# Kernel tuning notes

Hardware: AMD Instinct MI355X
Metric: run time of the kernel (lower is better)

The kernel has to match this reference:

```python
import jax, jax.numpy as jnp
import numpy as np
import math

D_RES, N_HEADS, D_HEAD, D_MLP = 1024, 16, 64, 4096
EPS = 1e-5
IGNORE = -100000.0


def setup_inputs() -> dict:
    key = jax.random.key(0)
    ks = jax.random.split(key, 8)
    std = 0.02
    return {
        "resid_pre": jax.random.normal(ks[0], (2, 2048, D_RES), dtype=jnp.float32),
        "ln1_w": jnp.ones((D_RES,), jnp.float32),
        "ln1_b": jnp.zeros((D_RES,), jnp.float32),
        "W_Q": jax.random.normal(ks[1], (N_HEADS, D_RES, D_HEAD), jnp.float32) * std,
        "b_Q": jnp.zeros((N_HEADS, D_HEAD), jnp.float32),
        "W_K": jax.random.normal(ks[2], (N_HEADS, D_RES, D_HEAD), jnp.float32) * std,
        "b_K": jnp.zeros((N_HEADS, D_HEAD), jnp.float32),
        "W_V": jax.random.normal(ks[3], (N_HEADS, D_RES, D_HEAD), jnp.float32) * std,
        "b_V": jnp.zeros((N_HEADS, D_HEAD), jnp.float32),
        "W_O": jax.random.normal(ks[4], (N_HEADS, D_HEAD, D_RES), jnp.float32) * std,
        "b_O": jnp.zeros((D_RES,), jnp.float32),
        "ln2_w": jnp.ones((D_RES,), jnp.float32),
        "ln2_b": jnp.zeros((D_RES,), jnp.float32),
        "W_in": jax.random.normal(ks[5], (D_RES, D_MLP), jnp.float32) * std,
        "b_in": jnp.zeros((D_MLP,), jnp.float32),
        "W_out": jax.random.normal(ks[6], (D_MLP, D_RES), jnp.float32) * std,
        "b_out": jnp.zeros((D_RES,), jnp.float32),
    }


def _layernorm(x, w, b):
    x = x - jnp.mean(x, axis=-1, keepdims=True)
    scale = jnp.sqrt(jnp.mean(x * x, axis=-1, keepdims=True) + EPS)
    return (x / scale) * w + b


def reference(resid_pre, ln1_w, ln1_b, W_Q, b_Q, W_K, b_K, W_V, b_V, W_O, b_O,
              ln2_w, ln2_b, W_in, b_in, W_out, b_out):
    x = _layernorm(resid_pre, ln1_w, ln1_b)  # [b,s,d]
    q = jnp.einsum('bsd,hde->bshe', x, W_Q) + b_Q
    k = jnp.einsum('bsd,hde->bshe', x, W_K) + b_K
    v = jnp.einsum('bsd,hde->bshe', x, W_V) + b_V
    scores = jnp.einsum('bqhe,bkhe->bhqk', q, k) / math.sqrt(D_HEAD)
    S = scores.shape[-1]
    mask = jnp.triu(jnp.ones((S, S), dtype=bool), k=1)
    scores = jnp.where(mask, IGNORE, scores)
    pattern = jax.nn.softmax(scores, axis=-1)
    z = jnp.einsum('bhqk,bkhe->bqhe', pattern, v)
    attn_out = jnp.einsum('bqhe,hed->bqd', z, W_O) + b_O
    resid_mid = resid_pre + attn_out
    y = _layernorm(resid_mid, ln2_w, ln2_b)
    pre = jnp.einsum('bsd,dm->bsm', y, W_in) + b_in
    post = jax.nn.gelu(pre, approximate=False)
    mlp_out = jnp.einsum('bsm,md->bsd', post, W_out) + b_out
    return resid_mid + mlp_out
```

## Files before the change

kernel.cpp:

```cpp
#include <hip/hip_runtime.h>
#include <cstddef>

typedef unsigned short u16;
using short8 = __attribute__((ext_vector_type(8))) short;
using f32x4  = __attribute__((ext_vector_type(4))) float;

__device__ __forceinline__ float bf2f(u16 u) {
  union { unsigned int i; float f; } v; v.i = ((unsigned int)u) << 16; return v.f;
}
__device__ __forceinline__ u16 f2bf(float f) {
  __bf16 h = (__bf16)f;
  return __builtin_bit_cast(unsigned short, h);
}

__device__ __forceinline__ void load_lds16(const u16* g, u16* l) {
  __builtin_amdgcn_global_load_lds((const __attribute__((address_space(1))) void*)g,
                                   (__attribute__((address_space(3))) void*)l, 16, 0, 0);
}

__global__ __launch_bounds__(256) void prep_k(const float* __restrict__ wq,
                                              const float* __restrict__ wk,
                                              const float* __restrict__ wv,
                                              const float* __restrict__ wo,
                                              const float* __restrict__ win,
                                              const float* __restrict__ wout,
                                              const float* __restrict__ bq,
                                              const float* __restrict__ bk,
                                              const float* __restrict__ bv,
                                              u16* __restrict__ wqkvT,
                                              u16* __restrict__ woT,
                                              u16* __restrict__ winT,
                                              u16* __restrict__ woutT,
                                              float* __restrict__ qkvBias) {
  __shared__ float tile[32][33];
  int id = blockIdx.x;
  int tx = threadIdx.x, ty = threadIdx.y;

  if (id == 12288) {
    int t = ty * 32 + tx;
#pragma unroll
    for (int i = 0; i < 12; ++i) {
      int idx = i * 256 + t;
      float v = (idx < 1024) ? bq[idx] : (idx < 2048) ? bk[idx - 1024] : bv[idx - 2048];
      qkvBias[idx] = v;
    }
    return;
  }

  const float* in; u16* out; int R, C, c0, r0;
  if (id < 3072) {
    int s = id >> 10, r = id & 1023;
    int h = r >> 6, tt = r & 63;
    const float* W = (s == 0) ? wq : (s == 1) ? wk : wv;
    in = W + h * 65536;
    out = wqkvT + (size_t)s * 1024 * 1024 + h * 64 * 1024;
    R = 1024; C = 64;
    c0 = (tt & 1) * 32; r0 = (tt >> 1) * 32;
  } else if (id < 4096) {
    int tt = id - 3072;
    in = wo; out = woT; R = 1024; C = 1024;
    c0 = (tt & 31) * 32; r0 = (tt >> 5) * 32;
  } else if (id < 8192) {
    int tt = id - 4096;
    in = win; out = winT; R = 1024; C = 4096;
    c0 = (tt & 127) * 32; r0 = (tt >> 7) * 32;
  } else {
    int tt = id - 8192;
    in = wout; out = woutT; R = 4096; C = 1024;
    c0 = (tt & 31) * 32; r0 = (tt >> 5) * 32;
  }

#pragma unroll
  for (int i = 0; i < 32; i += 8)
    tile[ty + i][tx] = in[(size_t)(r0 + ty + i) * C + c0 + tx];
  __syncthreads();
#pragma unroll
  for (int i = 0; i < 32; i += 8)
    out[(size_t)(c0 + ty + i) * R + r0 + tx] = f2bf(tile[tx][ty + i]);
}

__global__ __launch_bounds__(256) void transpose_v_k(const u16* __restrict__ qkv,
                                                     u16* __restrict__ vT) {
  __shared__ u16 tile[32][33];
  int bh = blockIdx.z;
  int b = bh >> 4, h = bh & 15;
  const u16* in = qkv + (size_t)b * 2048 * 3072 + 2048 + h * 64;
  u16* out = vT + (size_t)bh * 64 * 2048;
  int e0 = blockIdx.x * 32, s0 = blockIdx.y * 32;
  int tx = threadIdx.x, ty = threadIdx.y;
#pragma unroll
  for (int i = 0; i < 32; i += 8)
    tile[ty + i][tx] = in[(size_t)(s0 + ty + i) * 3072 + e0 + tx];
  __syncthreads();
#pragma unroll
  for (int i = 0; i < 32; i += 8)
    out[(size_t)(e0 + ty + i) * 2048 + s0 + tx] = tile[tx][ty + i];
}

__global__ __launch_bounds__(256) void ln_k(const float* __restrict__ inp,
                                            const float* __restrict__ w,
                                            const float* __restrict__ bias,
                                            u16* __restrict__ out) {
  __shared__ float red[2][4];
  int row = blockIdx.x, t = threadIdx.x;
  int wave = t >> 6, lane = t & 63;
  size_t base = (size_t)row * 1024 + t * 4;
  float4 f = *(const float4*)(inp + base);
  float v[4] = {f.x, f.y, f.z, f.w};
  float s = v[0] + v[1] + v[2] + v[3];
#pragma unroll
  for (int off = 32; off; off >>= 1) s += __shfl_xor(s, off, 64);
  if (lane == 0) red[0][wave] = s;
  __syncthreads();
  float mean = (red[0][0] + red[0][1] + red[0][2] + red[0][3]) * (1.f / 1024.f);
  float c[4]; float sq = 0.f;
#pragma unroll
  for (int j = 0; j < 4; ++j) { c[j] = v[j] - mean; sq += c[j] * c[j]; }
#pragma unroll
  for (int off = 32; off; off >>= 1) sq += __shfl_xor(sq, off, 64);
  if (lane == 0) red[1][wave] = sq;
  __syncthreads();
  float var = (red[1][0] + red[1][1] + red[1][2] + red[1][3]) * (1.f / 1024.f);
  float inv = 1.f / sqrtf(var + 1e-5f);
  float4 wv = *(const float4*)(w + t * 4);
  float4 bv = *(const float4*)(bias + t * 4);
  out[base + 0] = f2bf(c[0] * inv * wv.x + bv.x);
  out[base + 1] = f2bf(c[1] * inv * wv.y + bv.y);
  out[base + 2] = f2bf(c[2] * inv * wv.z + bv.z);
  out[base + 3] = f2bf(c[3] * inv * wv.w + bv.w);
}

template<int TN, bool RESIDF, bool GELU, bool OUTF32>
__global__ __launch_bounds__(256, 2) void gemm_k(const u16* __restrict__ A,
                                                 const u16* __restrict__ BT,
                                                 const float* __restrict__ bias,
                                                 const float* __restrict__ resid,
                                                 void* __restrict__ Cout,
                                                 int M, int N, int K) {
  constexpr int NS = TN / 32;
  __shared__ u16 As[128 * 64];
  __shared__ u16 Bs[TN * 64];
  int n0 = blockIdx.x * TN, m0 = blockIdx.y * 128;
  int t = threadIdx.x;
  int wave = t >> 6, lane = t & 63;
  int wr = wave >> 1, wc = wave & 1;
  int ln16 = lane & 15, quad = lane >> 4;

  f32x4 acc[4][NS];
#pragma unroll
  for (int i = 0; i < 4; ++i)
#pragma unroll
    for (int j = 0; j < NS; ++j) acc[i][j] = (f32x4){0.f, 0.f, 0.f, 0.f};

  int lrow8 = lane >> 3;
  int gseg  = (lane & 7) ^ lrow8;
  const u16* aG = A  + (size_t)(m0 + wave * 8 + lrow8) * K + gseg * 8;
  const u16* bG = BT + (size_t)(n0 + wave * 8 + lrow8) * K + gseg * 8;
  u16* aL = As + wave * 8 * 64;
  u16* bL = Bs + wave * 8 * 64;

  int e = ln16 & 7;
  int arow = wr * 64 + ln16;
  int brow = wc * (TN / 2) + ln16;

  for (int k0 = 0; k0 < K; k0 += 64) {
    __syncthreads();
#pragma unroll
    for (int i = 0; i < 4; ++i)
      load_lds16(aG + (size_t)i * 32 * K + k0, aL + i * 32 * 64);
#pragma unroll
    for (int i = 0; i < TN / 32; ++i)
      load_lds16(bG + (size_t)i * 32 * K + k0, bL + i * 32 * 64);
    __syncthreads();
#pragma unroll
    for (int kk = 0; kk < 2; ++kk) {
      int slot = (kk * 4 + quad) ^ e;
      short8 af[4], bf[NS];
#pragma unroll
      for (int ms = 0; ms < 4; ++ms)
        af[ms] = *(const short8*)&As[(arow + ms * 16) * 64 + slot * 8];
#pragma unroll
      for (int ns = 0; ns < NS; ++ns)
        bf[ns] = *(const short8*)&Bs[(brow + ns * 16) * 64 + slot * 8];
#pragma unroll
      for (int ms = 0; ms < 4; ++ms)
#pragma unroll
        for (int ns = 0; ns < NS; ++ns)
          acc[ms][ns] = __builtin_amdgcn_mfma_f32_16x16x32_bf16(af[ms], bf[ns], acc[ms][ns], 0, 0, 0);
    }
  }

#pragma unroll
  for (int ms = 0; ms < 4; ++ms)
#pragma unroll
    for (int ns = 0; ns < NS; ++ns)
#pragma unroll
      for (int r = 0; r < 4; ++r) {
        int grow = m0 + wr * 64 + ms * 16 + quad * 4 + r;
        int gcol = n0 + wc * (TN / 2) + ns * 16 + ln16;
        size_t idx = (size_t)grow * N + gcol;
        float v = acc[ms][ns][r] + bias[gcol];
        if (GELU) v = 0.5f * v * (1.f + erff(v * 0.70710678118654752f));
        if (RESIDF) v += resid[idx];
        if (OUTF32) ((float*)Cout)[idx] = v;
        else        ((u16*)Cout)[idx] = f2bf(v);
      }
}

__global__ __launch_bounds__(256) void attn_k(const u16* __restrict__ qkv,
                                              const u16* __restrict__ vT,
                                              u16* __restrict__ z) {
  __shared__ u16 Ks[64 * 64];
  __shared__ u16 Vs[64 * 64];
  __shared__ u16 Ps[2][4][16][72];
  int pair = blockIdx.x, h = blockIdx.y, b = blockIdx.z;
  int qtA = pair, qtB = 31 - pair;
  int t = threadIdx.x, wave = t >> 6, lane = t & 63;
  int ln16 = lane & 15, quad = lane >> 4;

  int qbase[2] = {qtA * 64 + wave * 16, qtB * 64 + wave * 16};
  short8 aq[2][2];
#pragma unroll
  for (int i = 0; i < 2; ++i) {
    const u16* qrow = qkv + (size_t)(b * 2048 + qbase[i] + ln16) * 3072 + h * 64;
    aq[i][0] = *(const short8*)(qrow + quad * 8);
    aq[i][1] = *(const short8*)(qrow + 32 + quad * 8);
  }

  f32x4 zero4 = {0.f, 0.f, 0.f, 0.f};
  f32x4 o[2][4];
  float l_i[2][4];
#pragma unroll
  for (int i = 0; i < 2; ++i)
#pragma unroll
    for (int n = 0; n < 4; ++n) { o[i][n] = zero4; l_i[i][n] = 0.f; }

  int lrow = lane >> 3;
  int gseg = (lane & 7) ^ lrow;
  const u16* kB = qkv + (size_t)(b * 2048 + wave * 16 + lrow) * 3072 + 1024 + h * 64 + gseg * 8;
  const u16* vB = vT + ((size_t)(b * 16 + h) * 64 + wave * 16 + lrow) * 2048 + gseg * 8;
  u16* kL = Ks + wave * 16 * 64;
  u16* vL = Vs + wave * 16 * 64;

  const float SC = 0.125f * 1.44269504088896340736f;
  int e = ln16 & 7;
  int nkt = qtB + 1;
  for (int kt = 0; kt < nkt; ++kt) {
    __syncthreads();
    size_t kOff = (size_t)kt * 64 * 3072;
    size_t vOff = (size_t)kt * 64;
#pragma unroll
    for (int i = 0; i < 2; ++i) {
      load_lds16(kB + kOff + (size_t)i * 8 * 3072, kL + i * 8 * 64);
      load_lds16(vB + vOff + (size_t)i * 8 * 2048, vL + i * 8 * 64);
    }
    __syncthreads();

    int kg = kt * 64;
#pragma unroll
    for (int i = 0; i < 2; ++i) {
      if (i == 0 && kt > qtA) continue;
      f32x4 s[4] = {zero4, zero4, zero4, zero4};
#pragma unroll
      for (int kk = 0; kk < 2; ++kk) {
        short8 a = aq[i][kk];
        int slot = (kk * 4 + quad) ^ e;
#pragma unroll
        for (int n = 0; n < 4; ++n) {
          short8 kb = *(const short8*)&Ks[(n * 16 + ln16) * 64 + slot * 8];
          s[n] = __builtin_amdgcn_mfma_f32_16x16x32_bf16(a, kb, s[n], 0, 0, 0);
        }
      }
#pragma unroll
      for (int r = 0; r < 4; ++r) {
        int gq = qbase[i] + quad * 4 + r;
        float sum = 0.f;
#pragma unroll
        for (int n = 0; n < 4; ++n) {
          float p = (kg + n * 16 + ln16 > gq) ? 0.f : exp2f(s[n][r] * SC);
          sum += p;
          Ps[i][wave][quad * 4 + r][n * 16 + ln16] = f2bf(p);
        }
#pragma unroll
        for (int off = 8; off; off >>= 1) sum += __shfl_xor(sum, off, 16);
        l_i[i][r] += sum;
      }
#pragma unroll
      for (int kk = 0; kk < 2; ++kk) {
        short8 ap = *(const short8*)&Ps[i][wave][ln16][kk * 32 + quad * 8];
        int slot = (kk * 4 + quad) ^ e;
#pragma unroll
        for (int n = 0; n < 4; ++n) {
          short8 bv = *(const short8*)&Vs[(n * 16 + ln16) * 64 + slot * 8];
          o[i][n] = __builtin_amdgcn_mfma_f32_16x16x32_bf16(ap, bv, o[i][n], 0, 0, 0);
        }
      }
    }
  }

#pragma unroll
  for (int i = 0; i < 2; ++i) {
    float inv[4];
#pragma unroll
    for (int r = 0; r < 4; ++r) inv[r] = 1.f / l_i[i][r];
#pragma unroll
    for (int n = 0; n < 4; ++n)
#pragma unroll
      for (int r = 0; r < 4; ++r)
        z[(size_t)(b * 2048 + qbase[i] + quad * 4 + r) * 1024 + h * 64 + n * 16 + ln16] =
            f2bf(o[i][n][r] * inv[r]);
  }
}

extern "C" void kernel_launch(void* const* d_in, const int* in_sizes, int n_in,
                              void* d_out, int out_size, void* d_ws, size_t ws_size,
                              hipStream_t stream) {
  const float* resid_pre = (const float*)d_in[0];
  const float* ln1_w = (const float*)d_in[1];
  const float* ln1_b = (const float*)d_in[2];
  const float* W_Q  = (const float*)d_in[3];
  const float* b_Q  = (const float*)d_in[4];
  const float* W_K  = (const float*)d_in[5];
  const float* b_K  = (const float*)d_in[6];
  const float* W_V  = (const float*)d_in[7];
  const float* b_V  = (const float*)d_in[8];
  const float* W_O  = (const float*)d_in[9];
  const float* b_O  = (const float*)d_in[10];
  const float* ln2_w = (const float*)d_in[11];
  const float* ln2_b = (const float*)d_in[12];
  const float* W_in  = (const float*)d_in[13];
  const float* b_in  = (const float*)d_in[14];
  const float* W_out = (const float*)d_in[15];
  const float* b_out = (const float*)d_in[16];
  float* out = (float*)d_out;

  char* w = (char*)d_ws;
  u16* WqkvT = (u16*)w;  w += (size_t)3072 * 1024 * 2;
  u16* WoT   = (u16*)w;  w += (size_t)1024 * 1024 * 2;
  u16* WinT  = (u16*)w;  w += (size_t)4096 * 1024 * 2;
  u16* WoutT = (u16*)w;  w += (size_t)1024 * 4096 * 2;
  float* qkvBias = (float*)w; w += 3072 * 4;
  u16* xln   = (u16*)w;  w += (size_t)4096 * 1024 * 2;
  float* resid_mid = (float*)w; w += (size_t)4096 * 1024 * 4;
  u16* qkvBuf = (u16*)w; w += (size_t)4096 * 3072 * 2;
  u16* zBuf  = (u16*)w;  w += (size_t)4096 * 1024 * 2;
  u16* vTBuf = (u16*)w;  w += (size_t)32 * 64 * 2048 * 2;
  u16* hBuf  = qkvBuf;

  dim3 tb(32, 8);
  prep_k<<<12289, tb, 0, stream>>>(W_Q, W_K, W_V, W_O, W_in, W_out,
                                   b_Q, b_K, b_V,
                                   WqkvT, WoT, WinT, WoutT, qkvBias);

  ln_k<<<4096, 256, 0, stream>>>(resid_pre, ln1_w, ln1_b, xln);
  gemm_k<128, false, false, false><<<dim3(24, 32), 256, 0, stream>>>(
      xln, WqkvT, qkvBias, nullptr, qkvBuf, 4096, 3072, 1024);
  transpose_v_k<<<dim3(2, 64, 32), tb, 0, stream>>>(qkvBuf, vTBuf);
  attn_k<<<dim3(16, 16, 2), 256, 0, stream>>>(qkvBuf, vTBuf, zBuf);
  gemm_k<64, true, false, true><<<dim3(16, 32), 256, 0, stream>>>(
      zBuf, WoT, b_O, resid_pre, resid_mid, 4096, 1024, 1024);
  ln_k<<<4096, 256, 0, stream>>>(resid_mid, ln2_w, ln2_b, xln);
  gemm_k<128, false, true, false><<<dim3(32, 32), 256, 0, stream>>>(
      xln, WinT, b_in, nullptr, hBuf, 4096, 4096, 1024);
  gemm_k<64, true, false, true><<<dim3(16, 32), 256, 0, stream>>>(
      hBuf, WoutT, b_out, resid_mid, out, 4096, 1024, 4096);
}
```

Baseline: 367.6 us.

## Split attention KV loop and N=1024 GEMMs across blocks with merge kernels

Attention now divides each query tile's key loop between two blocks, interleaving key tiles by parity. Partial outputs and row sums are written to scratch and combined in a new merge kernel. The two N=1024 GEMMs (W_O and W_out) now use split-K with two bf16 partial buffers. Merge kernels add bias and residual, and the first merge is fused with LayerNorm 2. The goal is to fill more CUs, since the previous grids were small (512 blocks for GEMMs, 512 for attention). The cost is extra launches and partial-buffer traffic, plus precision loss from rounding partials to bf16.

```diff
diff --git a/kernel.cpp b/kernel.cpp
--- a/kernel.cpp
+++ b/kernel.cpp
@@ -130,17 +130,83 @@
   out[base + 3] = f2bf(c[3] * inv * wv.w + bv.w);
 }
 
-template<int TN, bool RESIDF, bool GELU, bool OUTF32>
+__global__ __launch_bounds__(256) void merge_ln_k(const u16* __restrict__ p,
+                                                  const float* __restrict__ bO,
+                                                  const float* __restrict__ resid_pre,
+                                                  float* __restrict__ resid_mid,
+                                                  const float* __restrict__ w,
+                                                  const float* __restrict__ bias,
+                                                  u16* __restrict__ out) {
+  __shared__ float red[2][4];
+  const size_t S = (size_t)4096 * 1024;
+  int row = blockIdx.x, t = threadIdx.x;
+  int wave = t >> 6, lane = t & 63;
+  size_t base = (size_t)row * 1024 + t * 4;
+  float4 f = *(const float4*)(resid_pre + base);
+  float4 bo = *(const float4*)(bO + t * 4);
+  ushort4 a0 = *(const ushort4*)(p + base);
+  ushort4 a1 = *(const ushort4*)(p + S + base);
+  float v[4];
+  v[0] = f.x + bo.x + bf2f(a0.x) + bf2f(a1.x);
+  v[1] = f.y + bo.y + bf2f(a0.y) + bf2f(a1.y);
+  v[2] = f.z + bo.z + bf2f(a0.z) + bf2f(a1.z);
+  v[3] = f.w + bo.w + bf2f(a0.w) + bf2f(a1.w);
+  *(float4*)(resid_mid + base) = (float4){v[0], v[1], v[2], v[3]};
+  float s = v[0] + v[1] + v[2] + v[3];
+#pragma unroll
+  for (int off = 32; off; off >>= 1) s += __shfl_xor(s, off, 64);
+  if (lane == 0) red[0][wave] = s;
+  __syncthreads();
+  float mean = (red[0][0] + red[0][1] + red[0][2] + red[0][3]) * (1.f / 1024.f);
+  float c[4]; float sq = 0.f;
+#pragma unroll
+  for (int j = 0; j < 4; ++j) { c[j] = v[j] - mean; sq += c[j] * c[j]; }
+#pragma unroll
+  for (int off = 32; off; off >>= 1) sq += __shfl_xor(sq, off, 64);
+  if (lane == 0) red[1][wave] = sq;
+  __syncthreads();
+  float var = (red[1][0] + red[1][1] + red[1][2] + red[1][3]) * (1.f / 1024.f);
+  float inv = 1.f / sqrtf(var + 1e-5f);
+  float4 wv = *(const float4*)(w + t * 4);
+  float4 bv = *(const float4*)(bias + t * 4);
+  out[base + 0] = f2bf(c[0] * inv * wv.x + bv.x);
+  out[base + 1] = f2bf(c[1] * inv * wv.y + bv.y);
+  out[base + 2] = f2bf(c[2] * inv * wv.z + bv.z);
+  out[base + 3] = f2bf(c[3] * inv * wv.w + bv.w);
+}
+
+__global__ __launch_bounds__(256) void merge_out_k(const u16* __restrict__ p,
+                                                   const float* __restrict__ bout,
+                                                   const float* __restrict__ resid_mid,
+                                                   float* __restrict__ out) {
+  const size_t S = (size_t)4096 * 1024;
+  int row = blockIdx.x, t = threadIdx.x;
+  size_t base = (size_t)row * 1024 + t * 4;
+  float4 f = *(const float4*)(resid_mid + base);
+  float4 bo = *(const float4*)(bout + t * 4);
+  ushort4 a0 = *(const ushort4*)(p + base);
+  ushort4 a1 = *(const ushort4*)(p + S + base);
+  float4 r;
+  r.x = f.x + bo.x + bf2f(a0.x) + bf2f(a1.x);
+  r.y = f.y + bo.y + bf2f(a0.y) + bf2f(a1.y);
+  r.z = f.z + bo.z + bf2f(a0.z) + bf2f(a1.z);
+  r.w = f.w + bo.w + bf2f(a0.w) + bf2f(a1.w);
+  *(float4*)(out + base) = r;
+}
+
+template<int TN, bool RESIDF, bool GELU, bool OUTF32, bool SPLIT>
 __global__ __launch_bounds__(256, 2) void gemm_k(const u16* __restrict__ A,
                                                  const u16* __restrict__ BT,
                                                  const float* __restrict__ bias,
                                                  const float* __restrict__ resid,
                                                  void* __restrict__ Cout,
-                                                 int M, int N, int K) {
+                                                 int M, int N, int K,
+                                                 int lda, int ldb) {
   constexpr int NS = TN / 32;
   __shared__ u16 As[128 * 64];
   __shared__ u16 Bs[TN * 64];
   int n0 = blockIdx.x * TN, m0 = blockIdx.y * 128;
+  int koff = SPLIT ? blockIdx.z * K : 0;
   int t = threadIdx.x;
   int wave = t >> 6, lane = t & 63;
   int wr = wave >> 1, wc = wave & 1;
@@ -154,8 +220,8 @@
 
   int lrow8 = lane >> 3;
   int gseg  = (lane & 7) ^ lrow8;
-  const u16* aG = A  + (size_t)(m0 + wave * 8 + lrow8) * K + gseg * 8;
-  const u16* bG = BT + (size_t)(n0 + wave * 8 + lrow8) * K + gseg * 8;
+  const u16* aG = A  + (size_t)(m0 + wave * 8 + lrow8) * lda + koff + gseg * 8;
+  const u16* bG = BT + (size_t)(n0 + wave * 8 + lrow8) * ldb + koff + gseg * 8;
   u16* aL = As + wave * 8 * 64;
   u16* bL = Bs + wave * 8 * 64;
 
@@ -167,10 +233,10 @@
     __syncthreads();
 #pragma unroll
     for (int i = 0; i < 4; ++i)
-      load_lds16(aG + (size_t)i * 32 * K + k0, aL + i * 32 * 64);
+      load_lds16(aG + (size_t)i * 32 * lda + k0, aL + i * 32 * 64);
 #pragma unroll
     for (int i = 0; i < TN / 32; ++i)
-      load_lds16(bG + (size_t)i * 32 * K + k0, bL + i * 32 * 64);
+      load_lds16(bG + (size_t)i * 32 * ldb + k0, bL + i * 32 * 64);
     __syncthreads();
 #pragma unroll
     for (int kk = 0; kk < 2; ++kk) {
@@ -190,6 +256,7 @@
     }
   }
 
+  u16* part = SPLIT ? ((u16*)Cout + (size_t)blockIdx.z * M * N) : nullptr;
 #pragma unroll
   for (int ms = 0; ms < 4; ++ms)
 #pragma unroll
@@ -199,26 +266,32 @@
         int grow = m0 + wr * 64 + ms * 16 + quad * 4 + r;
         int gcol = n0 + wc * (TN / 2) + ns * 16 + ln16;
         size_t idx = (size_t)grow * N + gcol;
-        float v = acc[ms][ns][r] + bias[gcol];
-        if (GELU) v = 0.5f * v * (1.f + erff(v * 0.70710678118654752f));
-        if (RESIDF) v += resid[idx];
-        if (OUTF32) ((float*)Cout)[idx] = v;
-        else        ((u16*)Cout)[idx] = f2bf(v);
+        if (SPLIT) {
+          part[idx] = f2bf(acc[ms][ns][r]);
+        } else {
+          float v = acc[ms][ns][r] + bias[gcol];
+          if (GELU) v = 0.5f * v * (1.f + erff(v * 0.70710678118654752f));
+          if (RESIDF) v += resid[idx];
+          if (OUTF32) ((float*)Cout)[idx] = v;
+          else        ((u16*)Cout)[idx] = f2bf(v);
+        }
       }
 }
 
 __global__ __launch_bounds__(256) void attn_k(const u16* __restrict__ qkv,
                                               const u16* __restrict__ vT,
-                                              u16* __restrict__ z) {
+                                              u16* __restrict__ oPart,
+                                              float* __restrict__ lPart) {
   __shared__ u16 Ks[64 * 64];
   __shared__ u16 Vs[64 * 64];
   __shared__ u16 Ps[2][4][16][72];
-  int pair = blockIdx.x, h = blockIdx.y, b = blockIdx.z;
-  int qtA = pair, qtB = 31 - pair;
+  int pair = blockIdx.x, h = blockIdx.y;
+  int b = blockIdx.z >> 1, s = blockIdx.z & 1;
+  int qtT[2] = {pair, 31 - pair};
   int t = threadIdx.x, wave = t >> 6, lane = t & 63;
   int ln16 = lane & 15, quad = lane >> 4;
 
-  int qbase[2] = {qtA * 64 + wave * 16, qtB * 64 + wave * 16};
+  int qbase[2] = {qtT[0] * 64 + wave * 16, qtT[1] * 64 + wave * 16};
   short8 aq[2][2];
 #pragma unroll
   for (int i = 0; i < 2; ++i) {
@@ -244,8 +317,8 @@
 
   const float SC = 0.125f * 1.44269504088896340736f;
   int e = ln16 & 7;
-  int nkt = qtB + 1;
-  for (int kt = 0; kt < nkt; ++kt) {
+  int nkt = qtT[1] + 1;
+  for (int kt = s; kt < nkt; kt += 2) {
     __syncthreads();
     size_t kOff = (size_t)kt * 64 * 3072;
     size_t vOff = (size_t)kt * 64;
@@ -259,8 +332,8 @@
     int kg = kt * 64;
 #pragma unroll
     for (int i = 0; i < 2; ++i) {
-      if (i == 0 && kt > qtA) continue;
-      f32x4 s[4] = {zero4, zero4, zero4, zero4};
+      if (i == 0 && kt > qtT[0]) continue;
+      f32x4 sreg[4] = {zero4, zero4, zero4, zero4};
 #pragma unroll
       for (int kk = 0; kk < 2; ++kk) {
         short8 a = aq[i][kk];
@@ -268,7 +341,7 @@
 #pragma unroll
         for (int n = 0; n < 4; ++n) {
           short8 kb = *(const short8*)&Ks[(n * 16 + ln16) * 64 + slot * 8];
-          s[n] = __builtin_amdgcn_mfma_f32_16x16x32_bf16(a, kb, s[n], 0, 0, 0);
+          sreg[n] = __builtin_amdgcn_mfma_f32_16x16x32_bf16(a, kb, sreg[n], 0, 0, 0);
         }
       }
 #pragma unroll
@@ -277,7 +350,7 @@
         float sum = 0.f;
 #pragma unroll
         for (int n = 0; n < 4; ++n) {
-          float p = (kg + n * 16 + ln16 > gq) ? 0.f : exp2f(s[n][r] * SC);
+          float p = (kg + n * 16 + ln16 > gq) ? 0.f : exp2f(sreg[n][r] * SC);
           sum += p;
           Ps[i][wave][quad * 4 + r][n * 16 + ln16] = f2bf(p);
         }
@@ -300,16 +373,43 @@
 
 #pragma unroll
   for (int i = 0; i < 2; ++i) {
-    float inv[4];
-#pragma unroll
-    for (int r = 0; r < 4; ++r) inv[r] = 1.f / l_i[i][r];
+    size_t base = ((((size_t)(s * 2 + b) * 16 + h) * 32 + qtT[i]) * 64);
 #pragma unroll
     for (int n = 0; n < 4; ++n)
 #pragma unroll
+      for (int r = 0; r < 4; ++r) {
+        int row = wave * 16 + quad * 4 + r;
+        oPart[(base + row) * 64 + n * 16 + ln16] = f2bf(o[i][n][r]);
+      }
+    if (ln16 == 0)
+#pragma unroll
       for (int r = 0; r < 4; ++r)
-        z[(size_t)(b * 2048 + qbase[i] + quad * 4 + r) * 1024 + h * 64 + n * 16 + ln16] =
-            f2bf(o[i][n][r] * inv[r]);
-  }
+        lPart[base + wave * 16 + quad * 4 + r] = l_i[i][r];
+  }
+}
+
+__global__ __launch_bounds__(256) void merge_attn_k(const u16* __restrict__ oPart,
+                                                    const float* __restrict__ lPart,
+                                                    u16* __restrict__ z) {
+  const size_t S = (size_t)2 * 16 * 32 * 64 * 64;
+  const size_t L = (size_t)2 * 16 * 32 * 64;
+  unsigned tid = blockIdx.x * 256 + threadIdx.x;
+  int c4  = tid & 15;
+  int row = (tid >> 4) & 63;
+  int qt  = (tid >> 10) & 31;
+  int h   = (tid >> 15) & 15;
+  int b   = tid >> 19;
+  size_t lIdx = (((size_t)(b * 16 + h) * 32 + qt) * 64 + row);
+  size_t pIdx = lIdx * 64 + c4 * 4;
+  float inv = 1.f / (lPart[lIdx] + lPart[L + lIdx]);
+  ushort4 a0 = *(const ushort4*)(oPart + pIdx);
+  ushort4 a1 = *(const ushort4*)(oPart + S + pIdx);
+  ushort4 r;
+  r.x = f2bf((bf2f(a0.x) + bf2f(a1.x)) * inv);
+  r.y = f2bf((bf2f(a0.y) + bf2f(a1.y)) * inv);
+  r.z = f2bf((bf2f(a0.z) + bf2f(a1.z)) * inv);
+  r.w = f2bf((bf2f(a0.w) + bf2f(a1.w)) * inv);
+  *(ushort4*)(z + (size_t)(b * 2048 + qt * 64 + row) * 1024 + h * 64 + c4 * 4) = r;
 }
 
 extern "C" void kernel_launch(void* const* d_in, const int* in_sizes, int n_in,
@@ -340,12 +440,16 @@
   u16* WinT  = (u16*)w;  w += (size_t)4096 * 1024 * 2;
   u16* WoutT = (u16*)w;  w += (size_t)1024 * 4096 * 2;
   float* qkvBias = (float*)w; w += 3072 * 4;
+  char* xr   = w;
   u16* xln   = (u16*)w;  w += (size_t)4096 * 1024 * 2;
   float* resid_mid = (float*)w; w += (size_t)4096 * 1024 * 4;
   u16* qkvBuf = (u16*)w; w += (size_t)4096 * 3072 * 2;
   u16* zBuf  = (u16*)w;  w += (size_t)4096 * 1024 * 2;
   u16* vTBuf = (u16*)w;  w += (size_t)32 * 64 * 2048 * 2;
+  u16* partP = (u16*)w;  w += (size_t)2 * 4096 * 1024 * 2;
   u16* hBuf  = qkvBuf;
+  u16*   oPart = (u16*)xr;
+  float* lPart = (float*)(xr + (size_t)2 * 2 * 16 * 32 * 64 * 64 * 2);
 
   dim3 tb(32, 8);
   prep_k<<<12289, tb, 0, stream>>>(W_Q, W_K, W_V, W_O, W_in, W_out,
@@ -353,15 +457,18 @@
                                    WqkvT, WoT, WinT, WoutT, qkvBias);
 
   ln_k<<<4096, 256, 0, stream>>>(resid_pre, ln1_w, ln1_b, xln);
-  gemm_k<128, false, false, false><<<dim3(24, 32), 256, 0, stream>>>(
-      xln, WqkvT, qkvBias, nullptr, qkvBuf, 4096, 3072, 1024);
+  gemm_k<128, false, false, false, false><<<dim3(24, 32), 256, 0, stream>>>(
+      xln, WqkvT, qkvBias, nullptr, qkvBuf, 4096, 3072, 1024, 1024, 1024);
   transpose_v_k<<<dim3(2, 64, 32), tb, 0, stream>>>(qkvBuf, vTBuf);
-  attn_k<<<dim3(16, 16, 2), 256, 0, stream>>>(qkvBuf, vTBuf, zBuf);
-  gemm_k<64, true, false, true><<<dim3(16, 32), 256, 0, stream>>>(
-      zBuf, WoT, b_O, resid_pre, resid_mid, 4096, 1024, 1024);
-  ln_k<<<4096, 256, 0, stream>>>(resid_mid, ln2_w, ln2_b, xln);
-  gemm_k<128, false, true, false><<<dim3(32, 32), 256, 0, stream>>>(
-      xln, WinT, b_in, nullptr, hBuf, 4096, 4096, 1024);
-  gemm_k<64, true, false, true><<<dim3(16, 32), 256, 0, stream>>>(
-      hBuf, WoutT, b_out, resid_mid, out, 4096, 1024, 4096);
-}
+  attn_k<<<dim3(16, 16, 4), 256, 0, stream>>>(qkvBuf, vTBuf, oPart, lPart);
+  merge_attn_k<<<4096, 256, 0, stream>>>(oPart, lPart, zBuf);
+  gemm_k<64, false, false, false, true><<<dim3(16, 32, 2), 256, 0, stream>>>(
+      zBuf, WoT, nullptr, nullptr, partP, 4096, 1024, 512, 1024, 1024);
+  merge_ln_k<<<4096, 256, 0, stream>>>(partP, b_O, resid_pre, resid_mid,
+                                       ln2_w, ln2_b, xln);
+  gemm_k<128, false, true, false, false><<<dim3(32, 32), 256, 0, stream>>>(
+      xln, WinT, b_in, nullptr, hBuf, 4096, 4096, 1024, 1024, 1024);
+  gemm_k<64, false, false, false, true><<<dim3(16, 32, 2), 256, 0, stream>>>(
+      hBuf, WoutT, nullptr, nullptr, partP, 4096, 1024, 2048, 4096, 4096);
+  merge_out_k<<<4096, 256, 0, stream>>>(partP, b_out, resid_mid, out);
+}
```

After: 371.1 us. Within noise of the previous version (+1.0%).
